# Kernel optimization log

Measured on AMD Instinct MI355X. Metric: run time of the kernel, lower is better.

The kernel has to match this reference:

```python
import jax, jax.numpy as jnp
import numpy as np
from jax import lax

D_MODEL = 1024
N_EXPERTS = 8
N_ACTIVE = 2
FFN_HIDDEN = int(D_MODEL * 2.0)


def setup_inputs() -> dict:
    key = jax.random.key(0)
    ks = jax.random.split(key, 7)
    B, T = 2, 2048
    s_in = 1.0 / np.sqrt(D_MODEL)
    s_h = 1.0 / np.sqrt(FFN_HIDDEN)
    return {
        "x": jax.random.normal(ks[0], (B, T, D_MODEL), dtype=jnp.float32),
        # router: torch Linear(d_model, n_experts, bias=False) weight [E, D]
        "router_w": jax.random.uniform(ks[1], (N_EXPERTS, D_MODEL), jnp.float32, -s_in, s_in),
        # stacked expert FFN params: w1 [E, H, D], b1 [E, H], w2 [E, D, H], b2 [E, D]
        "w1": jax.random.uniform(ks[2], (N_EXPERTS, FFN_HIDDEN, D_MODEL), jnp.float32, -s_in, s_in),
        "b1": jax.random.uniform(ks[3], (N_EXPERTS, FFN_HIDDEN), jnp.float32, -s_in, s_in),
        "w2": jax.random.uniform(ks[4], (N_EXPERTS, D_MODEL, FFN_HIDDEN), jnp.float32, -s_h, s_h),
        "b2": jax.random.uniform(ks[5], (N_EXPERTS, D_MODEL), jnp.float32, -s_h, s_h),
    }


def reference(x, router_w, w1, b1, w2, b2):
    B, T, D = x.shape
    N = B * T
    xf = x.reshape(N, D)

    logits = xf @ router_w.T                      # [N, E]
    probs = jax.nn.softmax(logits, axis=-1)       # [N, E]

    # --- aux load-balancing loss (f_i is non-differentiable, from indices) ---
    _, disp_idx = lax.top_k(logits, N_ACTIVE)     # [N, K]
    disp_mask = jax.nn.one_hot(disp_idx, N_EXPERTS, dtype=logits.dtype).sum(axis=1)  # [N, E]
    f_i = disp_mask.sum(axis=0) / (N * N_ACTIVE)  # [E]
    P_i = probs.mean(axis=0)                      # [E]
    aux_loss = N_EXPERTS * jnp.sum(f_i * P_i)

    # --- top-k combine weights, renormalized ---
    topk_w, topk_idx = lax.top_k(probs, N_ACTIVE)                 # [N, K]
    topk_w = topk_w / topk_w.sum(axis=-1, keepdims=True)
    # scatter top-k weights into dense [N, E] combine matrix (zeros elsewhere)
    combine_w = (jax.nn.one_hot(topk_idx, N_EXPERTS, dtype=xf.dtype) * topk_w[..., None]).sum(axis=1)

    # --- expert FFNs, weighted combine (loop over small fixed expert set) ---
    out = jnp.zeros_like(xf)
    for e in range(N_EXPERTS):
        h = jax.nn.silu(xf @ w1[e].T + b1[e])     # [N, H]
        y = h @ w2[e].T + b2[e]                   # [N, D]
        out = out + combine_w[:, e:e + 1] * y

    return out.reshape(B, T, D), aux_loss
```

## Files before the change

### kernel.cpp

```cpp
#include <hip/hip_runtime.h>
#include <cstdint>
#include <cstddef>

#define D_MODEL 1024
#define N_EXPERTS 8
#define FFN_H 2048
#define N_TOK 4096
#define CAP 2048

typedef float f32x4 __attribute__((ext_vector_type(4)));
typedef __bf16 bf16x8 __attribute__((ext_vector_type(8)));

static constexpr size_t XB_OFF   = 0;
static constexpr size_t W1B_OFF  = XB_OFF  + (size_t)N_TOK * D_MODEL * 2;
static constexpr size_t W2B_OFF  = W1B_OFF + (size_t)N_EXPERTS * FFN_H * D_MODEL * 2;
static constexpr size_t HBUF_OFF = W2B_OFF + (size_t)N_EXPERTS * D_MODEL * FFN_H * 2;
static constexpr size_t YBUF_OFF = HBUF_OFF + (size_t)N_EXPERTS * CAP * FFN_H * 2;
static constexpr size_t CNT_OFF  = YBUF_OFF + (size_t)N_EXPERTS * CAP * D_MODEL * 2;
static constexpr size_t PSUM_OFF = CNT_OFF + 32;
static constexpr size_t TOK_OFF  = PSUM_OFF + 32;
static constexpr size_t TIX_OFF  = TOK_OFF + (size_t)N_EXPERTS * CAP * 4;
static constexpr size_t TIW_OFF  = TIX_OFF + (size_t)N_TOK * 8;

__device__ __forceinline__ void async_ld16(const void* g, void* l) {
    __builtin_amdgcn_global_load_lds(
        (const __attribute__((address_space(1))) unsigned int*)g,
        (__attribute__((address_space(3))) unsigned int*)l, 16, 0, 0);
}

__global__ __launch_bounds__(256) void prep_kernel(const float* __restrict__ x,
                                                   const float* __restrict__ rw,
                                                   const float* __restrict__ w1,
                                                   const float* __restrict__ w2,
                                                   __bf16* __restrict__ xb,
                                                   __bf16* __restrict__ w1b,
                                                   __bf16* __restrict__ w2b,
                                                   int* __restrict__ counts,
                                                   float* __restrict__ psum,
                                                   int* __restrict__ tok_list,
                                                   int2* __restrict__ tinfo_idx,
                                                   float2* __restrict__ tinfo_w) {
    __shared__ float rws[N_EXPERTS * D_MODEL];
    __shared__ int s_e0[64], s_e1[64], s_r0[64], s_r1[64];
    __shared__ float s_w0[64], s_w1[64];
    __shared__ int hist[8], base[8];
    __shared__ float pacc[8];

    int tid = threadIdx.x;
    int b = blockIdx.x;
    if (b >= 64) {
        int c = b - 64;
        const float* src; __bf16* dst; size_t bb;
        if (c < 2048)       { src = x;  dst = xb;  bb = (size_t)c * 2048; }
        else if (c < 10240) { src = w1; dst = w1b; bb = (size_t)(c - 2048) * 2048; }
        else                { src = w2; dst = w2b; bb = (size_t)(c - 10240) * 2048; }
        size_t i = bb + (size_t)tid * 8;
        float4 a = *reinterpret_cast<const float4*>(src + i);
        float4 d = *reinterpret_cast<const float4*>(src + i + 4);
        bf16x8 r;
        r[0] = (__bf16)a.x; r[1] = (__bf16)a.y; r[2] = (__bf16)a.z; r[3] = (__bf16)a.w;
        r[4] = (__bf16)d.x; r[5] = (__bf16)d.y; r[6] = (__bf16)d.z; r[7] = (__bf16)d.w;
        *reinterpret_cast<bf16x8*>(dst + i) = r;
        return;
    }

    for (int i = tid * 4; i < N_EXPERTS * D_MODEL; i += 256 * 4)
        *reinterpret_cast<float4*>(&rws[i]) = *reinterpret_cast<const float4*>(&rw[i]);
    if (tid < 8) { hist[tid] = 0; pacc[tid] = 0.f; }
    __syncthreads();

    int wave = tid >> 6, lane = tid & 63;
    float psacc[8] = {};
    for (int it = 0; it < 16; ++it) {
        int li = wave * 16 + it;
        int t = b * 64 + li;
        const float* xr = x + (size_t)t * D_MODEL;
        float acc[8] = {};
#pragma unroll
        for (int i = 0; i < D_MODEL / 64; ++i) {
            float xv = xr[lane + 64 * i];
#pragma unroll
            for (int e = 0; e < 8; ++e) acc[e] += xv * rws[e * D_MODEL + lane + 64 * i];
        }
        float logit[8];
#pragma unroll
        for (int e = 0; e < 8; ++e) {
            float v = acc[e];
            for (int off = 32; off; off >>= 1) v += __shfl_xor(v, off);
            logit[e] = v;
        }
        float mx = logit[0];
#pragma unroll
        for (int e = 1; e < 8; ++e) mx = fmaxf(mx, logit[e]);
        float p[8], s = 0.f;
#pragma unroll
        for (int e = 0; e < 8; ++e) { p[e] = expf(logit[e] - mx); s += p[e]; }
        float inv = 1.f / s;
#pragma unroll
        for (int e = 0; e < 8; ++e) { p[e] *= inv; psacc[e] += p[e]; }
        int e0 = 0; float p0 = p[0];
#pragma unroll
        for (int e = 1; e < 8; ++e) if (p[e] > p0) { p0 = p[e]; e0 = e; }
        int e1 = -1; float p1 = -1.f;
#pragma unroll
        for (int e = 0; e < 8; ++e) if (e != e0 && p[e] > p1) { p1 = p[e]; e1 = e; }
        float invw = 1.f / (p0 + p1);
        if (lane == 0) {
            s_e0[li] = e0; s_e1[li] = e1;
            s_w0[li] = p0 * invw; s_w1[li] = p1 * invw;
        }
    }
    if (lane == 0)
#pragma unroll
        for (int e = 0; e < 8; ++e) atomicAdd(&pacc[e], psacc[e]);
    __syncthreads();

    if (tid < 64) {
        s_r0[tid] = atomicAdd(&hist[s_e0[tid]], 1);
        s_r1[tid] = atomicAdd(&hist[s_e1[tid]], 1);
    }
    __syncthreads();
    if (tid < 8) {
        base[tid] = atomicAdd(&counts[tid], hist[tid]);
        atomicAdd(&psum[tid], pacc[tid]);
    }
    __syncthreads();
    if (tid < 64) {
        int t = b * 64 + tid;
        int e0 = s_e0[tid], e1 = s_e1[tid];
        int q0 = min(base[e0] + s_r0[tid], CAP - 1);
        int q1 = min(base[e1] + s_r1[tid], CAP - 1);
        tok_list[e0 * CAP + q0] = t;
        tok_list[e1 * CAP + q1] = t;
        tinfo_idx[t] = make_int2(e0 * CAP + q0, e1 * CAP + q1);
        tinfo_w[t] = make_float2(s_w0[tid], s_w1[tid]);
    }
}

template <int KDIM, bool PASS2>
__global__ __launch_bounds__(256, 4) void ffn_kernel(const __bf16* __restrict__ A_base,
                                                     const __bf16* __restrict__ B_base,
                                                     const float* __restrict__ bias,
                                                     const int* __restrict__ counts,
                                                     const int* __restrict__ tok_list,
                                                     __bf16* __restrict__ Out_base) {
    constexpr int BROWS = PASS2 ? D_MODEL : FFN_H;
    constexpr int NT = BROWS / 128;
    int bid = blockIdx.x;
    int e = bid & 7;
    int r = bid >> 3;
    int n0 = (r % NT) * 128;
    int m0 = (r / NT) * 128;
    int cnt = min(counts[e], CAP);
    if (m0 >= cnt) return;

    __shared__ __bf16 s_a[2][128 * 32];
    __shared__ __bf16 s_b[2][128 * 32];
    __shared__ int s_tok[128];

    int tid = threadIdx.x;
    if (!PASS2 && tid < 128) {
        int slot = min(m0 + tid, cnt - 1);
        s_tok[tid] = tok_list[e * CAP + slot];
    }
    __syncthreads();

    int colk = (tid & 3) * 8;
    const __bf16 *a_src0, *a_src1;
    if (PASS2) {
        int s0 = min(m0 + (tid >> 2), cnt - 1);
        int s1 = min(m0 + 64 + (tid >> 2), cnt - 1);
        a_src0 = A_base + ((size_t)e * CAP + s0) * KDIM + colk;
        a_src1 = A_base + ((size_t)e * CAP + s1) * KDIM + colk;
    } else {
        a_src0 = A_base + (size_t)s_tok[tid >> 2] * KDIM + colk;
        a_src1 = A_base + (size_t)s_tok[64 + (tid >> 2)] * KDIM + colk;
    }
    const __bf16* b_src0 = B_base + ((size_t)e * BROWS + n0 + (tid >> 2)) * KDIM + colk;
    const __bf16* b_src1 = b_src0 + (size_t)64 * KDIM;

    char* lds_a = (char*)&s_a[0][0] + (tid >> 6) * 1024;
    char* lds_b = (char*)&s_b[0][0] + (tid >> 6) * 1024;

    int wv = tid >> 6, lane = tid & 63;
    int wm = wv >> 1, wn = wv & 1;
    int lm = lane & 15, q = lane >> 4;
    int a_base = (wm * 64 + lm) * 32 + q * 8;
    int b_base = (wn * 64 + lm) * 32 + q * 8;

    f32x4 acc[4][4] = {};
    for (int k0 = 0; k0 < KDIM; k0 += 64) {
        async_ld16(a_src0 + k0,      lds_a);
        async_ld16(a_src1 + k0,      lds_a + 4096);
        async_ld16(a_src0 + k0 + 32, lds_a + 8192);
        async_ld16(a_src1 + k0 + 32, lds_a + 8192 + 4096);
        async_ld16(b_src0 + k0,      lds_b);
        async_ld16(b_src1 + k0,      lds_b + 4096);
        async_ld16(b_src0 + k0 + 32, lds_b + 8192);
        async_ld16(b_src1 + k0 + 32, lds_b + 8192 + 4096);
        __syncthreads();
#pragma unroll
        for (int kk = 0; kk < 2; ++kk) {
            bf16x8 af[4], bf[4];
#pragma unroll
            for (int f = 0; f < 4; ++f) {
                af[f] = *reinterpret_cast<const bf16x8*>(&s_a[kk][a_base + f * 16 * 32]);
                bf[f] = *reinterpret_cast<const bf16x8*>(&s_b[kk][b_base + f * 16 * 32]);
            }
#pragma unroll
            for (int fm = 0; fm < 4; ++fm)
#pragma unroll
                for (int fn = 0; fn < 4; ++fn)
                    acc[fm][fn] = __builtin_amdgcn_mfma_f32_16x16x32_bf16(af[fm], bf[fn], acc[fm][fn], 0, 0, 0);
        }
        __syncthreads();
    }

#pragma unroll
    for (int fn = 0; fn < 4; ++fn) {
        int n = n0 + wn * 64 + fn * 16 + lm;
        float bv = bias[e * BROWS + n];
#pragma unroll
        for (int fm = 0; fm < 4; ++fm) {
            int rbase = wm * 64 + fm * 16 + q * 4;
#pragma unroll
            for (int i = 0; i < 4; ++i) {
                int row = rbase + i;
                int slot = m0 + row;
                if (slot < cnt) {
                    float v = acc[fm][fn][i] + bv;
                    if (!PASS2) {
                        float sv = v / (1.f + __expf(-v));
                        Out_base[((size_t)e * CAP + slot) * FFN_H + n] = (__bf16)sv;
                    } else {
                        Out_base[((size_t)e * CAP + slot) * D_MODEL + n] = (__bf16)v;
                    }
                }
            }
        }
    }
}

__global__ __launch_bounds__(256) void combine_kernel(const __bf16* __restrict__ ybuf,
                                                      const int2* __restrict__ tinfo_idx,
                                                      const float2* __restrict__ tinfo_w,
                                                      const int* __restrict__ counts,
                                                      const float* __restrict__ psum,
                                                      float* __restrict__ out) {
    int tid = threadIdx.x;
    if (blockIdx.x == 0 && tid == 0) {
        float s = 0.f;
#pragma unroll
        for (int e = 0; e < 8; ++e)
            s += ((float)counts[e] / (float)(N_TOK * 2)) * (psum[e] / (float)N_TOK);
        out[(size_t)N_TOK * D_MODEL] = 8.f * s;
    }
    int t = blockIdx.x * 2 + (tid >> 7);
    int d0 = (tid & 127) * 8;
    int2 ix = tinfo_idx[t];
    float2 w = tinfo_w[t];
    bf16x8 ya = *reinterpret_cast<const bf16x8*>(ybuf + (size_t)ix.x * D_MODEL + d0);
    bf16x8 yb = *reinterpret_cast<const bf16x8*>(ybuf + (size_t)ix.y * D_MODEL + d0);
    float4 o0, o1;
    o0.x = w.x * (float)ya[0] + w.y * (float)yb[0];
    o0.y = w.x * (float)ya[1] + w.y * (float)yb[1];
    o0.z = w.x * (float)ya[2] + w.y * (float)yb[2];
    o0.w = w.x * (float)ya[3] + w.y * (float)yb[3];
    o1.x = w.x * (float)ya[4] + w.y * (float)yb[4];
    o1.y = w.x * (float)ya[5] + w.y * (float)yb[5];
    o1.z = w.x * (float)ya[6] + w.y * (float)yb[6];
    o1.w = w.x * (float)ya[7] + w.y * (float)yb[7];
    float* op = out + (size_t)t * D_MODEL + d0;
    *reinterpret_cast<float4*>(op) = o0;
    *reinterpret_cast<float4*>(op + 4) = o1;
}

extern "C" void kernel_launch(void* const* d_in, const int* in_sizes, int n_in,
                              void* d_out, int out_size, void* d_ws, size_t ws_size,
                              hipStream_t stream) {
    const float* x  = (const float*)d_in[0];
    const float* rw = (const float*)d_in[1];
    const float* w1 = (const float*)d_in[2];
    const float* b1 = (const float*)d_in[3];
    const float* w2 = (const float*)d_in[4];
    const float* b2 = (const float*)d_in[5];
    float* out = (float*)d_out;

    char* ws = (char*)d_ws;
    __bf16* xb     = (__bf16*)(ws + XB_OFF);
    __bf16* w1b    = (__bf16*)(ws + W1B_OFF);
    __bf16* w2b    = (__bf16*)(ws + W2B_OFF);
    __bf16* hbuf   = (__bf16*)(ws + HBUF_OFF);
    __bf16* ybuf   = (__bf16*)(ws + YBUF_OFF);
    int*    counts = (int*)(ws + CNT_OFF);
    float*  psum   = (float*)(ws + PSUM_OFF);
    int*    tok    = (int*)(ws + TOK_OFF);
    int2*   tix    = (int2*)(ws + TIX_OFF);
    float2* tiw    = (float2*)(ws + TIW_OFF);

    hipMemsetAsync(ws + CNT_OFF, 0, 64, stream);

    prep_kernel<<<64 + 18432, 256, 0, stream>>>(x, rw, w1, w2, xb, w1b, w2b,
                                                counts, psum, tok, tix, tiw);

    ffn_kernel<D_MODEL, false><<<8 * (FFN_H / 128) * (CAP / 128), 256, 0, stream>>>(
        xb, w1b, b1, counts, tok, hbuf);
    ffn_kernel<FFN_H, true><<<8 * (D_MODEL / 128) * (CAP / 128), 256, 0, stream>>>(
        hbuf, w2b, b2, counts, tok, ybuf);

    combine_kernel<<<N_TOK / 2, 256, 0, stream>>>(ybuf, tix, tiw, counts, psum, out);
}
```

Measured before the change: 305.5 us.

## Stage FFN epilogue through LDS for coalesced stores, shrink k-step, fuse x cast into router

The FFN GEMM kernel now has a single LDS buffer and a K step of 32 instead of 64. This cuts shared memory per block so more blocks fit per CU, and the launch-bounds occupancy hint is dropped. The epilogue writes bias+SiLU results into a padded LDS tile in two halves, then each thread issues 16-byte coalesced global stores instead of scattered 2-byte stores. The x-to-bf16 cast moves into the router blocks, which removes 2048 prep blocks. The price is twice as many barrier-separated k iterations with less memory in flight per step, plus extra syncs in the epilogue.

```diff
diff --git a/kernel.cpp b/kernel.cpp
--- a/kernel.cpp
+++ b/kernel.cpp
@@ -51,9 +51,8 @@
     if (b >= 64) {
         int c = b - 64;
         const float* src; __bf16* dst; size_t bb;
-        if (c < 2048)       { src = x;  dst = xb;  bb = (size_t)c * 2048; }
-        else if (c < 10240) { src = w1; dst = w1b; bb = (size_t)(c - 2048) * 2048; }
-        else                { src = w2; dst = w2b; bb = (size_t)(c - 10240) * 2048; }
+        if (c < 8192) { src = w1; dst = w1b; bb = (size_t)c * 2048; }
+        else          { src = w2; dst = w2b; bb = (size_t)(c - 8192) * 2048; }
         size_t i = bb + (size_t)tid * 8;
         float4 a = *reinterpret_cast<const float4*>(src + i);
         float4 d = *reinterpret_cast<const float4*>(src + i + 4);
@@ -64,6 +63,18 @@
         return;
     }
 
+    {
+        size_t base_i = (size_t)b * 64 * D_MODEL;
+        for (int i = tid; i < 64 * D_MODEL / 8; i += 256) {
+            size_t off = base_i + (size_t)i * 8;
+            float4 a = *reinterpret_cast<const float4*>(x + off);
+            float4 d = *reinterpret_cast<const float4*>(x + off + 4);
+            bf16x8 r;
+            r[0] = (__bf16)a.x; r[1] = (__bf16)a.y; r[2] = (__bf16)a.z; r[3] = (__bf16)a.w;
+            r[4] = (__bf16)d.x; r[5] = (__bf16)d.y; r[6] = (__bf16)d.z; r[7] = (__bf16)d.w;
+            *reinterpret_cast<bf16x8*>(xb + off) = r;
+        }
+    }
     for (int i = tid * 4; i < N_EXPERTS * D_MODEL; i += 256 * 4)
         *reinterpret_cast<float4*>(&rws[i]) = *reinterpret_cast<const float4*>(&rw[i]);
     if (tid < 8) { hist[tid] = 0; pacc[tid] = 0.f; }
@@ -138,14 +149,16 @@
 }
 
 template <int KDIM, bool PASS2>
-__global__ __launch_bounds__(256, 4) void ffn_kernel(const __bf16* __restrict__ A_base,
-                                                     const __bf16* __restrict__ B_base,
-                                                     const float* __restrict__ bias,
-                                                     const int* __restrict__ counts,
-                                                     const int* __restrict__ tok_list,
-                                                     __bf16* __restrict__ Out_base) {
+__global__ __launch_bounds__(256) void ffn_kernel(const __bf16* __restrict__ A_base,
+                                                  const __bf16* __restrict__ B_base,
+                                                  const float* __restrict__ bias,
+                                                  const int* __restrict__ counts,
+                                                  const int* __restrict__ tok_list,
+                                                  __bf16* __restrict__ Out_base) {
     constexpr int BROWS = PASS2 ? D_MODEL : FFN_H;
+    constexpr int OSTRIDE = PASS2 ? D_MODEL : FFN_H;
     constexpr int NT = BROWS / 128;
+    constexpr int CSTR = 136;
     int bid = blockIdx.x;
     int e = bid & 7;
     int r = bid >> 3;
@@ -154,8 +167,7 @@
     int cnt = min(counts[e], CAP);
     if (m0 >= cnt) return;
 
-    __shared__ __bf16 s_a[2][128 * 32];
-    __shared__ __bf16 s_b[2][128 * 32];
+    __shared__ __bf16 s_buf[64 * CSTR];
     __shared__ int s_tok[128];
 
     int tid = threadIdx.x;
@@ -179,65 +191,68 @@
     const __bf16* b_src0 = B_base + ((size_t)e * BROWS + n0 + (tid >> 2)) * KDIM + colk;
     const __bf16* b_src1 = b_src0 + (size_t)64 * KDIM;
 
-    char* lds_a = (char*)&s_a[0][0] + (tid >> 6) * 1024;
-    char* lds_b = (char*)&s_b[0][0] + (tid >> 6) * 1024;
+    char* lds_a = (char*)s_buf + (tid >> 6) * 1024;
+    char* lds_b = (char*)s_buf + 8192 + (tid >> 6) * 1024;
 
     int wv = tid >> 6, lane = tid & 63;
     int wm = wv >> 1, wn = wv & 1;
     int lm = lane & 15, q = lane >> 4;
     int a_base = (wm * 64 + lm) * 32 + q * 8;
-    int b_base = (wn * 64 + lm) * 32 + q * 8;
+    int b_base = 4096 + (wn * 64 + lm) * 32 + q * 8;
 
     f32x4 acc[4][4] = {};
-    for (int k0 = 0; k0 < KDIM; k0 += 64) {
-        async_ld16(a_src0 + k0,      lds_a);
-        async_ld16(a_src1 + k0,      lds_a + 4096);
-        async_ld16(a_src0 + k0 + 32, lds_a + 8192);
-        async_ld16(a_src1 + k0 + 32, lds_a + 8192 + 4096);
-        async_ld16(b_src0 + k0,      lds_b);
-        async_ld16(b_src1 + k0,      lds_b + 4096);
-        async_ld16(b_src0 + k0 + 32, lds_b + 8192);
-        async_ld16(b_src1 + k0 + 32, lds_b + 8192 + 4096);
+    for (int k0 = 0; k0 < KDIM; k0 += 32) {
+        async_ld16(a_src0 + k0, lds_a);
+        async_ld16(a_src1 + k0, lds_a + 4096);
+        async_ld16(b_src0 + k0, lds_b);
+        async_ld16(b_src1 + k0, lds_b + 4096);
         __syncthreads();
-#pragma unroll
-        for (int kk = 0; kk < 2; ++kk) {
-            bf16x8 af[4], bf[4];
-#pragma unroll
-            for (int f = 0; f < 4; ++f) {
-                af[f] = *reinterpret_cast<const bf16x8*>(&s_a[kk][a_base + f * 16 * 32]);
-                bf[f] = *reinterpret_cast<const bf16x8*>(&s_b[kk][b_base + f * 16 * 32]);
-            }
-#pragma unroll
-            for (int fm = 0; fm < 4; ++fm)
-#pragma unroll
-                for (int fn = 0; fn < 4; ++fn)
-                    acc[fm][fn] = __builtin_amdgcn_mfma_f32_16x16x32_bf16(af[fm], bf[fn], acc[fm][fn], 0, 0, 0);
-        }
+        bf16x8 af[4], bf[4];
+#pragma unroll
+        for (int f = 0; f < 4; ++f) {
+            af[f] = *reinterpret_cast<const bf16x8*>(&s_buf[a_base + f * 16 * 32]);
+            bf[f] = *reinterpret_cast<const bf16x8*>(&s_buf[b_base + f * 16 * 32]);
+        }
+#pragma unroll
+        for (int fm = 0; fm < 4; ++fm)
+#pragma unroll
+            for (int fn = 0; fn < 4; ++fn)
+                acc[fm][fn] = __builtin_amdgcn_mfma_f32_16x16x32_bf16(af[fm], bf[fn], acc[fm][fn], 0, 0, 0);
         __syncthreads();
     }
 
 #pragma unroll
-    for (int fn = 0; fn < 4; ++fn) {
-        int n = n0 + wn * 64 + fn * 16 + lm;
-        float bv = bias[e * BROWS + n];
-#pragma unroll
-        for (int fm = 0; fm < 4; ++fm) {
-            int rbase = wm * 64 + fm * 16 + q * 4;
-#pragma unroll
-            for (int i = 0; i < 4; ++i) {
-                int row = rbase + i;
-                int slot = m0 + row;
-                if (slot < cnt) {
-                    float v = acc[fm][fn][i] + bv;
-                    if (!PASS2) {
-                        float sv = v / (1.f + __expf(-v));
-                        Out_base[((size_t)e * CAP + slot) * FFN_H + n] = (__bf16)sv;
-                    } else {
-                        Out_base[((size_t)e * CAP + slot) * D_MODEL + n] = (__bf16)v;
+    for (int h = 0; h < 2; ++h) {
+        if (wm == h) {
+#pragma unroll
+            for (int fn = 0; fn < 4; ++fn) {
+                int col = wn * 64 + fn * 16 + lm;
+                float bv = bias[e * BROWS + n0 + col];
+#pragma unroll
+                for (int fm = 0; fm < 4; ++fm) {
+                    int rloc = fm * 16 + q * 4;
+#pragma unroll
+                    for (int i = 0; i < 4; ++i) {
+                        float v = acc[fm][fn][i] + bv;
+                        if (!PASS2) v = v / (1.f + __expf(-v));
+                        s_buf[(rloc + i) * CSTR + col] = (__bf16)v;
                     }
                 }
             }
         }
+        __syncthreads();
+#pragma unroll
+        for (int j = 0; j < 4; ++j) {
+            int rloc = (tid >> 4) + j * 16;
+            int coloff = (tid & 15) * 8;
+            int slot = m0 + h * 64 + rloc;
+            if (slot < cnt) {
+                bf16x8 vv = *reinterpret_cast<const bf16x8*>(&s_buf[rloc * CSTR + coloff]);
+                *reinterpret_cast<bf16x8*>(
+                    Out_base + ((size_t)e * CAP + slot) * OSTRIDE + n0 + coloff) = vv;
+            }
+        }
+        __syncthreads();
     }
 }
 
@@ -300,7 +315,7 @@
 
     hipMemsetAsync(ws + CNT_OFF, 0, 64, stream);
 
-    prep_kernel<<<64 + 18432, 256, 0, stream>>>(x, rw, w1, w2, xb, w1b, w2b,
+    prep_kernel<<<64 + 16384, 256, 0, stream>>>(x, rw, w1, w2, xb, w1b, w2b,
                                                 counts, psum, tok, tix, tiw);
 
     ffn_kernel<D_MODEL, false><<<8 * (FFN_H / 128) * (CAP / 128), 256, 0, stream>>>(
```

Result: slower. 324.1 us (+6.1%).
